# Performance work log

Hardware: AMD Instinct MI355X
Metric: run time of the kernel (lower is better)

The kernel has to match this reference:

```python
import jax, jax.numpy as jnp
import numpy as np

N_NODES = 50000
N_EDGES = 1_600_000
IN_DIM = 128
HID = 64


def gcn_conv(x, src, dst, w, W, b, n):
    # PyG GCNConv(normalize=True, add_self_loops=True):
    # add self loops with weight 1, sym-normalize, x@W (no bias in lin), scatter-add, +bias
    loop = jnp.arange(n)
    s = jnp.concatenate([src, loop])
    d = jnp.concatenate([dst, loop])
    ww = jnp.concatenate([w, jnp.ones((n,), w.dtype)])
    deg = jax.ops.segment_sum(ww, d, num_segments=n)                 # [n]
    dis = jnp.where(deg > 0, jax.lax.rsqrt(deg), 0.0)                # deg^{-1/2}, inf->0
    norm = dis[s] * ww * dis[d]                                      # [E+n]
    h = x @ W                                                        # [n, out]
    msg = h[s] * norm[:, None]                                       # gather + scale
    out = jax.ops.segment_sum(msg, d, num_segments=n)                # scatter-add at dst
    return out + b


def setup_inputs() -> dict:
    key = jax.random.key(0)
    ks = jax.random.split(key, 9)
    X = jax.random.normal(ks[0], (N_NODES, IN_DIM), dtype=jnp.float32)
    edge_index = jax.random.randint(ks[1], (2, N_EDGES), 0, N_NODES, dtype=jnp.int64)
    edge_weight = jax.random.uniform(ks[2], (N_EDGES,), dtype=jnp.float32)
    s1 = 1.0 / np.sqrt(IN_DIM)
    s2 = 1.0 / np.sqrt(HID)
    W1 = jax.random.uniform(ks[3], (IN_DIM, HID), jnp.float32, -s1, s1)
    b1 = jax.random.uniform(ks[4], (HID,), jnp.float32, -s1, s1)
    W2 = jax.random.uniform(ks[5], (HID, HID), jnp.float32, -s2, s2)
    b2 = jax.random.uniform(ks[6], (HID,), jnp.float32, -s2, s2)
    Wl = jax.random.uniform(ks[7], (HID, 1), jnp.float32, -s2, s2)
    bl = jax.random.uniform(ks[8], (1,), jnp.float32, -s2, s2)
    return {"X": X, "edge_index": edge_index, "edge_weight": edge_weight,
            "W1": W1, "b1": b1, "W2": W2, "b2": b2, "Wl": Wl, "bl": bl}


def reference(X, edge_index, edge_weight, W1, b1, W2, b2, Wl, bl):
    n = X.shape[0]
    src, dst = edge_index[0], edge_index[1]
    h = jax.nn.relu(gcn_conv(X, src, dst, edge_weight, W1, b1, n))
    # F.dropout(p=0.2) is identity in eval mode
    h = jax.nn.relu(gcn_conv(h, src, dst, edge_weight, W2, b2, n))
    return jax.nn.sigmoid(h @ Wl + bl).squeeze(1)   # [n]
```

## Files before the change

### kernel.cpp

```cpp
#include <hip/hip_runtime.h>

typedef float f32x2 __attribute__((ext_vector_type(2)));

#define A2B 512
#define A2T 512
#define STG 3200

__device__ __forceinline__ long ld_idx(const void* idx, long pos, int is64) {
  return is64 ? (long)((const long long*)idx)[pos]
              : (long)((const int*)idx)[pos];
}

__device__ __forceinline__ int detect_is64(const void* idx) {
  const unsigned long long* p = (const unsigned long long*)idx;
  unsigned long long v = p[threadIdx.x & 63];
  return (__ballot((v >> 32) != 0ull) == 0ull) ? 1 : 0;
}

__device__ __forceinline__ uint4 pack16_fp8(const float* acc) {
  uint4 o;
  unsigned v;
  v = 0;
  v = __builtin_amdgcn_cvt_pk_fp8_f32(acc[0],  acc[1],  v, false);
  v = __builtin_amdgcn_cvt_pk_fp8_f32(acc[2],  acc[3],  v, true);
  o.x = v; v = 0;
  v = __builtin_amdgcn_cvt_pk_fp8_f32(acc[4],  acc[5],  v, false);
  v = __builtin_amdgcn_cvt_pk_fp8_f32(acc[6],  acc[7],  v, true);
  o.y = v; v = 0;
  v = __builtin_amdgcn_cvt_pk_fp8_f32(acc[8],  acc[9],  v, false);
  v = __builtin_amdgcn_cvt_pk_fp8_f32(acc[10], acc[11], v, true);
  o.z = v; v = 0;
  v = __builtin_amdgcn_cvt_pk_fp8_f32(acc[12], acc[13], v, false);
  v = __builtin_amdgcn_cvt_pk_fp8_f32(acc[14], acc[15], v, true);
  o.w = v;
  return o;
}

__global__ __launch_bounds__(256) void k_front(const void* __restrict__ idx,
                                               unsigned* __restrict__ histT,
                                               long E, int chunk, unsigned M,
                                               const float* __restrict__ X,
                                               const float* __restrict__ W1,
                                               unsigned char* __restrict__ h, int n) {
  __shared__ float smem[2048];
  const int t = threadIdx.x;
  if (blockIdx.x < A2B) {
    unsigned* cnt = (unsigned*)smem;
    const int b = blockIdx.x;
    const int is64 = detect_is64(idx);
    cnt[t] = 0;
    __syncthreads();
    const long e0 = (long)b * chunk;
    long e1 = e0 + chunk; if (e1 > E) e1 = E;
    for (long e = e0 + t; e < e1; e += 256) {
      unsigned d = (unsigned)ld_idx(idx, E + e, is64);
      atomicAdd(&cnt[__umulhi(d, M)], 1u);
    }
    __syncthreads();
    histT[(size_t)t * A2B + b] = cnt[t];
    return;
  }
  float* Ws = smem;
  for (int i = t; i < 2048; i += 256)
    ((float4*)Ws)[i] = ((const float4*)W1)[i];
  __syncthreads();
  int gid = (blockIdx.x - A2B) * 256 + t;
  int node = gid >> 2;
  int fg = (gid & 3) * 16;
  if (node >= n) return;
  const float4* xr4 = (const float4*)(X + (size_t)node * 128);
  float acc[16];
#pragma unroll
  for (int f = 0; f < 16; ++f) acc[f] = 0.0f;
  for (int k4 = 0; k4 < 32; ++k4) {
    float4 x = xr4[k4];
#pragma unroll
    for (int kk = 0; kk < 4; ++kk) {
      float xv = (kk == 0) ? x.x : (kk == 1) ? x.y : (kk == 2) ? x.z : x.w;
      const float4* wrow = (const float4*)(Ws + (k4 * 4 + kk) * 64 + fg);
#pragma unroll
      for (int f4 = 0; f4 < 4; ++f4) {
        float4 w = wrow[f4];
        acc[f4 * 4 + 0] = fmaf(xv, w.x, acc[f4 * 4 + 0]);
        acc[f4 * 4 + 1] = fmaf(xv, w.y, acc[f4 * 4 + 1]);
        acc[f4 * 4 + 2] = fmaf(xv, w.z, acc[f4 * 4 + 2]);
        acc[f4 * 4 + 3] = fmaf(xv, w.w, acc[f4 * 4 + 3]);
      }
    }
  }
  *(uint4*)(h + (size_t)node * 64 + fg) = pack16_fp8(acc);
}

__global__ __launch_bounds__(256) void k_colscan(const unsigned* __restrict__ histT,
                                                 unsigned* __restrict__ baseT,
                                                 unsigned* __restrict__ colsum) {
  __shared__ unsigned sh[256];
  const int k = blockIdx.x, t = threadIdx.x;
  const uint2 v = ((const uint2*)(histT + (size_t)k * A2B))[t];
  unsigned s = v.x + v.y;
  sh[t] = s;
  __syncthreads();
  for (int off = 1; off < 256; off <<= 1) {
    unsigned u = (t >= off) ? sh[t - off] : 0;
    __syncthreads();
    sh[t] += u;
    __syncthreads();
  }
  unsigned excl = sh[t] - s;
  uint2 o; o.x = excl; o.y = excl + v.x;
  ((uint2*)(baseT + (size_t)k * A2B))[t] = o;
  if (t == 255) colsum[k] = sh[255];
}

__global__ __launch_bounds__(A2T) void k_bucket(const void* __restrict__ idx,
                                                const float* __restrict__ w,
                                                const unsigned* __restrict__ baseT,
                                                const unsigned* __restrict__ colsum,
                                                uint2* __restrict__ recs,
                                                long E, int chunk, unsigned M) {
  __shared__ uint2 stage[STG];
  __shared__ unsigned cnt[256], lofs[256], lbase[256], bcol[256], scanb[256];
  const int b = blockIdx.x, t = threadIdx.x;
  const long e0 = (long)b * chunk;
  long e1 = e0 + chunk; if (e1 > E) e1 = E;
  const int m = (int)(e1 - e0);
  const int is64 = detect_is64(idx);
  if (t < 256) scanb[t] = colsum[t];
  __syncthreads();
  for (int off = 1; off < 256; off <<= 1) {
    unsigned u = 0;
    if (t < 256 && t >= off) u = scanb[t - off];
    __syncthreads();
    if (t < 256) scanb[t] += u;
    __syncthreads();
  }
  if (t < 256) {
    bcol[t] = (scanb[t] - colsum[t]) + baseT[(size_t)t * A2B + b];
    cnt[t] = 0;
  }
  __syncthreads();
  unsigned short dc[8]; unsigned char kc[8];
  int nk = 0;
  for (long e = e0 + t; e < e1; e += A2T, ++nk) {
    unsigned d = (unsigned)ld_idx(idx, E + e, is64);
    unsigned kb = __umulhi(d, M);
    dc[nk] = (unsigned short)d; kc[nk] = (unsigned char)kb;
    atomicAdd(&cnt[kb], 1u);
  }
  __syncthreads();
  if (t < 256) scanb[t] = cnt[t];
  __syncthreads();
  for (int off = 1; off < 256; off <<= 1) {
    unsigned u = 0;
    if (t < 256 && t >= off) u = scanb[t - off];
    __syncthreads();
    if (t < 256) scanb[t] += u;
    __syncthreads();
  }
  if (t < 256) { unsigned ex = scanb[t] - cnt[t]; lbase[t] = ex; lofs[t] = ex; }
  __syncthreads();
  nk = 0;
  for (long e = e0 + t; e < e1; e += A2T, ++nk) {
    unsigned s = (unsigned)ld_idx(idx, e, is64);
    float wv = w[e];
    unsigned kb = kc[nk];
    unsigned pos = atomicAdd(&lofs[kb], 1u);
    stage[pos] = make_uint2(s | ((unsigned)dc[nk] << 16), __float_as_uint(wv));
  }
  __syncthreads();
  for (int i = t; i < m; i += A2T) {
    uint2 r = stage[i];
    unsigned kb = __umulhi(r.x >> 16, M);
    recs[bcol[kb] + (unsigned)i - lbase[kb]] = r;
  }
}

__global__ __launch_bounds__(1024) void k_build(const uint2* __restrict__ recs,
                                                const unsigned* __restrict__ colsum,
                                                int* __restrict__ rowptr,
                                                float* __restrict__ dis,
                                                float2* __restrict__ edges,
                                                int n, int dwidth, long E) {
  __shared__ float wsum[256];
  __shared__ unsigned cnt[256], lofs[256], scanb[256];
  __shared__ int shr0, shr1;
  const int k = blockIdx.x, t = threadIdx.x;
  const int d0 = k * dwidth;
  if (t < 256) scanb[t] = colsum[t];
  __syncthreads();
  for (int off = 1; off < 256; off <<= 1) {
    unsigned u = 0;
    if (t < 256 && t >= off) u = scanb[t - off];
    __syncthreads();
    if (t < 256) scanb[t] += u;
    __syncthreads();
  }
  if (t == k) { shr1 = (int)scanb[t]; shr0 = (int)(scanb[t] - colsum[t]); }
  if (t < 256) { wsum[t] = 0.0f; cnt[t] = 0; }
  __syncthreads();
  const int r0 = shr0, r1 = shr1;
  const int m = r1 - r0;
  for (int i = t; i < m; i += 1024) {
    uint2 r = recs[r0 + i];
    int dl = (int)(r.x >> 16) - d0;
    atomicAdd(&cnt[dl], 1u);
    atomicAdd(&wsum[dl], __uint_as_float(r.y));
  }
  __syncthreads();
  if (t < 256) scanb[t] = cnt[t];
  __syncthreads();
  for (int off = 1; off < 256; off <<= 1) {
    unsigned u = 0;
    if (t < 256 && t >= off) u = scanb[t - off];
    __syncthreads();
    if (t < 256) scanb[t] += u;
    __syncthreads();
  }
  if (t < 256) {
    unsigned ex = scanb[t] - cnt[t];
    lofs[t] = (unsigned)r0 + ex;
    int d = d0 + t;
    if (t < dwidth && d < n) {
      rowptr[d] = r0 + (int)ex;
      dis[d] = rsqrtf(1.0f + wsum[t]);
    }
  }
  if (k == gridDim.x - 1 && t == 0) rowptr[n] = (int)E;
  __syncthreads();
  for (int i = t; i < m; i += 1024) {
    uint2 r = recs[r0 + i];
    unsigned pos = atomicAdd(&lofs[(int)(r.x >> 16) - d0], 1u);
    edges[pos] = make_float2(__uint_as_float(r.x & 0xffffu), __uint_as_float(r.y));
  }
}

__device__ __forceinline__ void gather_acc(const unsigned char* __restrict__ h,
                                           const float* __restrict__ dis,
                                           const float2* __restrict__ edges,
                                           int beg, int end, float s0,
                                           int half, int l32, int fl, int eg,
                                           float* acc) {
#pragma unroll
  for (int i = 0; i < 8; ++i) acc[i] = 0.0f;
  for (int base = beg; base < end; base += 32) {
    int m = end - base; if (m > 32) m = 32;
    float2 pk = (l32 < m) ? edges[base + l32] : make_float2(__int_as_float(0), 0.0f);
    float nrm = dis[__float_as_int(pk.x)] * pk.y * s0;
    int steps = (m + 3) >> 2;
    for (int s = 0; s < steps; ++s) {
      int j = half * 32 + s * 4 + eg;
      int   sj = __float_as_int(__shfl(pk.x, j));
      float nj = __shfl(nrm, j);
      uint2 hv = *(const uint2*)(h + (size_t)sj * 64 + fl * 8);
      f32x2 p0 = __builtin_amdgcn_cvt_pk_f32_fp8(hv.x, false);
      f32x2 p1 = __builtin_amdgcn_cvt_pk_f32_fp8(hv.x, true);
      f32x2 p2 = __builtin_amdgcn_cvt_pk_f32_fp8(hv.y, false);
      f32x2 p3 = __builtin_amdgcn_cvt_pk_f32_fp8(hv.y, true);
      acc[0] = fmaf(p0[0], nj, acc[0]);
      acc[1] = fmaf(p0[1], nj, acc[1]);
      acc[2] = fmaf(p1[0], nj, acc[2]);
      acc[3] = fmaf(p1[1], nj, acc[3]);
      acc[4] = fmaf(p2[0], nj, acc[4]);
      acc[5] = fmaf(p2[1], nj, acc[5]);
      acc[6] = fmaf(p3[0], nj, acc[6]);
      acc[7] = fmaf(p3[1], nj, acc[7]);
    }
  }
#pragma unroll
  for (int off = 8; off < 32; off <<= 1)
#pragma unroll
    for (int i = 0; i < 8; ++i) acc[i] += __shfl_xor(acc[i], off);
}

__device__ __forceinline__ void add_bias_self(const unsigned char* __restrict__ h,
                                              const float* __restrict__ b,
                                              int node, int fl, float s0, float* acc) {
  uint2 hv = *(const uint2*)(h + (size_t)node * 64 + fl * 8);
  f32x2 q0 = __builtin_amdgcn_cvt_pk_f32_fp8(hv.x, false);
  f32x2 q1 = __builtin_amdgcn_cvt_pk_f32_fp8(hv.x, true);
  f32x2 q2 = __builtin_amdgcn_cvt_pk_f32_fp8(hv.y, false);
  f32x2 q3 = __builtin_amdgcn_cvt_pk_f32_fp8(hv.y, true);
  float hs[8] = {q0[0], q0[1], q1[0], q1[1], q2[0], q2[1], q3[0], q3[1]};
  float4 bv0 = *(const float4*)(b + fl * 8);
  float4 bv1 = *(const float4*)(b + fl * 8 + 4);
  float bb[8] = {bv0.x, bv0.y, bv0.z, bv0.w, bv1.x, bv1.y, bv1.z, bv1.w};
  float s2 = s0 * s0;
#pragma unroll
  for (int i = 0; i < 8; ++i) acc[i] += bb[i] + hs[i] * s2;
}

__global__ __launch_bounds__(256) void k_gather_mid(const unsigned char* __restrict__ h,
                                                    const float* __restrict__ dis,
                                                    const float2* __restrict__ edges,
                                                    const int* __restrict__ rowptr,
                                                    const float* __restrict__ b1,
                                                    const float* __restrict__ W2,
                                                    unsigned char* __restrict__ h2, int n) {
  __shared__ float W2s[64 * 64];
  __shared__ float xs[8 * 64];
  const int t = threadIdx.x;
  for (int i = t; i < 1024; i += 256)
    ((float4*)W2s)[i] = ((const float4*)W2)[i];
  int lane = t & 63;
  int half = lane >> 5;
  int l32 = lane & 31;
  int fl = lane & 7;
  int eg = (lane >> 3) & 3;
  int nl = t >> 5;
  int node = blockIdx.x * 8 + nl;
  int beg = 0, end = 0; float s0 = 0.0f;
  if (node < n) { beg = rowptr[node]; end = rowptr[node + 1]; s0 = dis[node]; }
  float acc[8];
  gather_acc(h, dis, edges, beg, end, s0, half, l32, fl, eg, acc);
  if (node < n) {
    add_bias_self(h, b1, node, fl, s0, acc);
    if (eg == 0) {
#pragma unroll
      for (int i = 0; i < 8; ++i) xs[nl * 64 + fl * 8 + i] = fmaxf(acc[i], 0.0f);
    }
  }
  __syncthreads();
  int tl = l32;
  int node2 = blockIdx.x * 8 + (t >> 5);
  if (node2 >= n) return;
  const float* xrow = xs + (t >> 5) * 64;
  int f = tl * 2;
  float a0 = 0.0f, a1 = 0.0f;
#pragma unroll 8
  for (int k = 0; k < 64; ++k) {
    float xk = xrow[k];
    f32x2 wv = *(const f32x2*)(W2s + k * 64 + f);
    a0 = fmaf(xk, wv[0], a0);
    a1 = fmaf(xk, wv[1], a1);
  }
  unsigned v = __builtin_amdgcn_cvt_pk_fp8_f32(a0, a1, 0u, false);
  *(unsigned short*)(h2 + (size_t)node2 * 64 + f) = (unsigned short)v;
}

__global__ __launch_bounds__(256) void k_gather_fin(const unsigned char* __restrict__ h,
                                                    const float* __restrict__ dis,
                                                    const float2* __restrict__ edges,
                                                    const int* __restrict__ rowptr,
                                                    const float* __restrict__ b2,
                                                    const float* __restrict__ Wl,
                                                    const float* __restrict__ bl,
                                                    float* __restrict__ out, int n) {
  int lane = threadIdx.x & 63;
  int half = lane >> 5;
  int l32 = lane & 31;
  int fl = lane & 7;
  int eg = (lane >> 3) & 3;
  int node = blockIdx.x * 8 + (int)(threadIdx.x >> 5);
  if (node >= n) return;
  int beg = rowptr[node], end = rowptr[node + 1];
  float s0 = dis[node];
  float acc[8];
  gather_acc(h, dis, edges, beg, end, s0, half, l32, fl, eg, acc);
  add_bias_self(h, b2, node, fl, s0, acc);
  float4 wl0 = *(const float4*)(Wl + fl * 8);
  float4 wl1 = *(const float4*)(Wl + fl * 8 + 4);
  float wl[8] = {wl0.x, wl0.y, wl0.z, wl0.w, wl1.x, wl1.y, wl1.z, wl1.w};
  float v = 0.0f;
#pragma unroll
  for (int i = 0; i < 8; ++i) v += fmaxf(acc[i], 0.0f) * wl[i];
#pragma unroll
  for (int off = 1; off < 8; off <<= 1) v += __shfl_xor(v, off);
  if (l32 == 0) out[node] = 1.0f / (1.0f + expf(-(v + bl[0])));
}

extern "C" void kernel_launch(void* const* d_in, const int* in_sizes, int n_in,
                              void* d_out, int out_size, void* d_ws, size_t ws_size,
                              hipStream_t stream) {
  const float* X  = (const float*)d_in[0];
  const void*  EI = d_in[1];
  const float* EW = (const float*)d_in[2];
  const float* W1 = (const float*)d_in[3];
  const float* b1 = (const float*)d_in[4];
  const float* W2 = (const float*)d_in[5];
  const float* b2 = (const float*)d_in[6];
  const float* Wl = (const float*)d_in[7];
  const float* bl = (const float*)d_in[8];
  float* out = (float*)d_out;

  const int  n = in_sizes[0] / 128;
  const long E = (long)in_sizes[1] / 2;

  const int chunk  = (int)((E + A2B - 1) / A2B);
  const int dwidth = (n + 255) / 256;
  const unsigned M = (unsigned)((0x100000000ULL + (unsigned)dwidth - 1) / (unsigned)dwidth);

  auto align = [](size_t x) { return (x + 255) & ~(size_t)255; };
  char* ws = (char*)d_ws;
  size_t off = 0;
  float*         dis    = (float*)(ws + off);         off += align((size_t)n * 4);
  int*           rowptr = (int*)(ws + off);           off += align((size_t)(n + 1) * 4);
  unsigned*      colsum = (unsigned*)(ws + off);      off += align(256 * 4);
  unsigned*      histT  = (unsigned*)(ws + off);      off += align((size_t)A2B * 256 * 4);
  unsigned*      baseT  = (unsigned*)(ws + off);      off += align((size_t)A2B * 256 * 4);
  uint2*         recs   = (uint2*)(ws + off);         off += align((size_t)E * 8);
  float2*        edges  = (float2*)(ws + off);        off += align((size_t)E * 8);
  unsigned char* A      = (unsigned char*)(ws + off); off += align((size_t)n * 64);
  unsigned char* A2     = (unsigned char*)(ws + off); off += align((size_t)n * 64);

  const int nbW = (n + 7) / 8;
  const int nbG = (n * 4 + 255) / 256;

  k_front<<<A2B + nbG, dim3(256), 0, stream>>>(EI, histT, E, chunk, M, X, W1, A, n);
  k_colscan<<<256, 256, 0, stream>>>(histT, baseT, colsum);
  k_bucket<<<A2B, A2T, 0, stream>>>(EI, EW, baseT, colsum, recs, E, chunk, M);
  k_build<<<256, 1024, 0, stream>>>(recs, colsum, rowptr, dis, edges, n, dwidth, E);

  k_gather_mid<<<nbW, dim3(256), 0, stream>>>(A, dis, edges, rowptr, b1, W2, A2, n);
  k_gather_fin<<<nbW, dim3(256), 0, stream>>>(A2, dis, edges, rowptr, b2, Wl, bl, out, n);
}
```

Measured before the change: 211.7 us.

## Split layer-2 GEMM out of gather kernel into separate fp8 GEMM kernel

After: 218.2 us. +3.1%, slower.

```diff
diff --git a/kernel.cpp b/kernel.cpp
--- a/kernel.cpp
+++ b/kernel.cpp
@@ -294,47 +294,68 @@
                                                     const float2* __restrict__ edges,
                                                     const int* __restrict__ rowptr,
                                                     const float* __restrict__ b1,
-                                                    const float* __restrict__ W2,
-                                                    unsigned char* __restrict__ h2, int n) {
-  __shared__ float W2s[64 * 64];
-  __shared__ float xs[8 * 64];
-  const int t = threadIdx.x;
-  for (int i = t; i < 1024; i += 256)
-    ((float4*)W2s)[i] = ((const float4*)W2)[i];
-  int lane = t & 63;
+                                                    unsigned char* __restrict__ x1, int n) {
+  int lane = threadIdx.x & 63;
   int half = lane >> 5;
   int l32 = lane & 31;
   int fl = lane & 7;
   int eg = (lane >> 3) & 3;
-  int nl = t >> 5;
-  int node = blockIdx.x * 8 + nl;
-  int beg = 0, end = 0; float s0 = 0.0f;
-  if (node < n) { beg = rowptr[node]; end = rowptr[node + 1]; s0 = dis[node]; }
+  int node = blockIdx.x * 8 + (int)(threadIdx.x >> 5);
+  if (node >= n) return;
+  int beg = rowptr[node], end = rowptr[node + 1];
+  float s0 = dis[node];
   float acc[8];
   gather_acc(h, dis, edges, beg, end, s0, half, l32, fl, eg, acc);
-  if (node < n) {
+  if (eg == 0) {
     add_bias_self(h, b1, node, fl, s0, acc);
-    if (eg == 0) {
-#pragma unroll
-      for (int i = 0; i < 8; ++i) xs[nl * 64 + fl * 8 + i] = fmaxf(acc[i], 0.0f);
+#pragma unroll
+    for (int i = 0; i < 8; ++i) acc[i] = fmaxf(acc[i], 0.0f);
+    unsigned w0 = 0, w1 = 0;
+    w0 = __builtin_amdgcn_cvt_pk_fp8_f32(acc[0], acc[1], w0, false);
+    w0 = __builtin_amdgcn_cvt_pk_fp8_f32(acc[2], acc[3], w0, true);
+    w1 = __builtin_amdgcn_cvt_pk_fp8_f32(acc[4], acc[5], w1, false);
+    w1 = __builtin_amdgcn_cvt_pk_fp8_f32(acc[6], acc[7], w1, true);
+    *(uint2*)(x1 + (size_t)node * 64 + fl * 8) = make_uint2(w0, w1);
+  }
+}
+
+__global__ __launch_bounds__(256) void k_gemm2b(const unsigned char* __restrict__ x1,
+                                                const float* __restrict__ W2,
+                                                unsigned char* __restrict__ h2, int n) {
+  __shared__ float Ws[64 * 64];
+  for (int i = threadIdx.x; i < 1024; i += 256)
+    ((float4*)Ws)[i] = ((const float4*)W2)[i];
+  __syncthreads();
+  int gid = blockIdx.x * 256 + threadIdx.x;
+  int node = gid >> 2;
+  int fg = (gid & 3) * 16;
+  if (node >= n) return;
+  const uint4* xr = (const uint4*)(x1 + (size_t)node * 64);
+  uint4 rw[4] = {xr[0], xr[1], xr[2], xr[3]};
+  const unsigned* words = (const unsigned*)rw;
+  float acc[16];
+#pragma unroll
+  for (int f = 0; f < 16; ++f) acc[f] = 0.0f;
+#pragma unroll 4
+  for (int w = 0; w < 16; ++w) {
+    f32x2 a = __builtin_amdgcn_cvt_pk_f32_fp8(words[w], false);
+    f32x2 c = __builtin_amdgcn_cvt_pk_f32_fp8(words[w], true);
+    float xv4[4] = {a[0], a[1], c[0], c[1]};
+#pragma unroll
+    for (int j = 0; j < 4; ++j) {
+      float xv = xv4[j];
+      const float4* wrow = (const float4*)(Ws + (w * 4 + j) * 64 + fg);
+#pragma unroll
+      for (int f4 = 0; f4 < 4; ++f4) {
+        float4 wv = wrow[f4];
+        acc[f4 * 4 + 0] = fmaf(xv, wv.x, acc[f4 * 4 + 0]);
+        acc[f4 * 4 + 1] = fmaf(xv, wv.y, acc[f4 * 4 + 1]);
+        acc[f4 * 4 + 2] = fmaf(xv, wv.z, acc[f4 * 4 + 2]);
+        acc[f4 * 4 + 3] = fmaf(xv, wv.w, acc[f4 * 4 + 3]);
+      }
     }
   }
-  __syncthreads();
-  int tl = l32;
-  int node2 = blockIdx.x * 8 + (t >> 5);
-  if (node2 >= n) return;
-  const float* xrow = xs + (t >> 5) * 64;
-  int f = tl * 2;
-  float a0 = 0.0f, a1 = 0.0f;
-#pragma unroll 8
-  for (int k = 0; k < 64; ++k) {
-    float xk = xrow[k];
-    f32x2 wv = *(const f32x2*)(W2s + k * 64 + f);
-    a0 = fmaf(xk, wv[0], a0);
-    a1 = fmaf(xk, wv[1], a1);
-  }
-  unsigned v = __builtin_amdgcn_cvt_pk_fp8_f32(a0, a1, 0u, false);
-  *(unsigned short*)(h2 + (size_t)node2 * 64 + f) = (unsigned short)v;
+  *(uint4*)(h2 + (size_t)node * 64 + fg) = pack16_fp8(acc);
 }
 
 __global__ __launch_bounds__(256) void k_gather_fin(const unsigned char* __restrict__ h,
@@ -400,6 +421,7 @@
   uint2*         recs   = (uint2*)(ws + off);         off += align((size_t)E * 8);
   float2*        edges  = (float2*)(ws + off);        off += align((size_t)E * 8);
   unsigned char* A      = (unsigned char*)(ws + off); off += align((size_t)n * 64);
+  unsigned char* X1     = (unsigned char*)(ws + off); off += align((size_t)n * 64);
   unsigned char* A2     = (unsigned char*)(ws + off); off += align((size_t)n * 64);
 
   const int nbW = (n + 7) / 8;
@@ -410,6 +432,7 @@
   k_bucket<<<A2B, A2T, 0, stream>>>(EI, EW, baseT, colsum, recs, E, chunk, M);
   k_build<<<256, 1024, 0, stream>>>(recs, colsum, rowptr, dis, edges, n, dwidth, E);
 
-  k_gather_mid<<<nbW, dim3(256), 0, stream>>>(A, dis, edges, rowptr, b1, W2, A2, n);
+  k_gather_mid<<<nbW, dim3(256), 0, stream>>>(A, dis, edges, rowptr, b1, X1, n);
+  k_gemm2b<<<nbG, dim3(256), 0, stream>>>(X1, W2, A2, n);
   k_gather_fin<<<nbW, dim3(256), 0, stream>>>(A2, dis, edges, rowptr, b2, Wl, bl, out, n);
 }
```

## Reorder second GCN layer to aggregate first then apply W2

Applied to the files above, without the earlier changes.

Result: slower. 221.3 us (+4.5%).

```diff
diff --git a/kernel.cpp b/kernel.cpp
--- a/kernel.cpp
+++ b/kernel.cpp
@@ -272,21 +272,17 @@
     for (int i = 0; i < 8; ++i) acc[i] += __shfl_xor(acc[i], off);
 }
 
-__device__ __forceinline__ void add_bias_self(const unsigned char* __restrict__ h,
-                                              const float* __restrict__ b,
-                                              int node, int fl, float s0, float* acc) {
+__device__ __forceinline__ void add_self(const unsigned char* __restrict__ h,
+                                         int node, int fl, float s0, float* acc) {
   uint2 hv = *(const uint2*)(h + (size_t)node * 64 + fl * 8);
   f32x2 q0 = __builtin_amdgcn_cvt_pk_f32_fp8(hv.x, false);
   f32x2 q1 = __builtin_amdgcn_cvt_pk_f32_fp8(hv.x, true);
   f32x2 q2 = __builtin_amdgcn_cvt_pk_f32_fp8(hv.y, false);
   f32x2 q3 = __builtin_amdgcn_cvt_pk_f32_fp8(hv.y, true);
   float hs[8] = {q0[0], q0[1], q1[0], q1[1], q2[0], q2[1], q3[0], q3[1]};
-  float4 bv0 = *(const float4*)(b + fl * 8);
-  float4 bv1 = *(const float4*)(b + fl * 8 + 4);
-  float bb[8] = {bv0.x, bv0.y, bv0.z, bv0.w, bv1.x, bv1.y, bv1.z, bv1.w};
   float s2 = s0 * s0;
 #pragma unroll
-  for (int i = 0; i < 8; ++i) acc[i] += bb[i] + hs[i] * s2;
+  for (int i = 0; i < 8; ++i) acc[i] += hs[i] * s2;
 }
 
 __global__ __launch_bounds__(256) void k_gather_mid(const unsigned char* __restrict__ h,
@@ -294,57 +290,7 @@
                                                     const float2* __restrict__ edges,
                                                     const int* __restrict__ rowptr,
                                                     const float* __restrict__ b1,
-                                                    const float* __restrict__ W2,
-                                                    unsigned char* __restrict__ h2, int n) {
-  __shared__ float W2s[64 * 64];
-  __shared__ float xs[8 * 64];
-  const int t = threadIdx.x;
-  for (int i = t; i < 1024; i += 256)
-    ((float4*)W2s)[i] = ((const float4*)W2)[i];
-  int lane = t & 63;
-  int half = lane >> 5;
-  int l32 = lane & 31;
-  int fl = lane & 7;
-  int eg = (lane >> 3) & 3;
-  int nl = t >> 5;
-  int node = blockIdx.x * 8 + nl;
-  int beg = 0, end = 0; float s0 = 0.0f;
-  if (node < n) { beg = rowptr[node]; end = rowptr[node + 1]; s0 = dis[node]; }
-  float acc[8];
-  gather_acc(h, dis, edges, beg, end, s0, half, l32, fl, eg, acc);
-  if (node < n) {
-    add_bias_self(h, b1, node, fl, s0, acc);
-    if (eg == 0) {
-#pragma unroll
-      for (int i = 0; i < 8; ++i) xs[nl * 64 + fl * 8 + i] = fmaxf(acc[i], 0.0f);
-    }
-  }
-  __syncthreads();
-  int tl = l32;
-  int node2 = blockIdx.x * 8 + (t >> 5);
-  if (node2 >= n) return;
-  const float* xrow = xs + (t >> 5) * 64;
-  int f = tl * 2;
-  float a0 = 0.0f, a1 = 0.0f;
-#pragma unroll 8
-  for (int k = 0; k < 64; ++k) {
-    float xk = xrow[k];
-    f32x2 wv = *(const f32x2*)(W2s + k * 64 + f);
-    a0 = fmaf(xk, wv[0], a0);
-    a1 = fmaf(xk, wv[1], a1);
-  }
-  unsigned v = __builtin_amdgcn_cvt_pk_fp8_f32(a0, a1, 0u, false);
-  *(unsigned short*)(h2 + (size_t)node2 * 64 + f) = (unsigned short)v;
-}
-
-__global__ __launch_bounds__(256) void k_gather_fin(const unsigned char* __restrict__ h,
-                                                    const float* __restrict__ dis,
-                                                    const float2* __restrict__ edges,
-                                                    const int* __restrict__ rowptr,
-                                                    const float* __restrict__ b2,
-                                                    const float* __restrict__ Wl,
-                                                    const float* __restrict__ bl,
-                                                    float* __restrict__ out, int n) {
+                                                    unsigned char* __restrict__ x1, int n) {
   int lane = threadIdx.x & 63;
   int half = lane >> 5;
   int l32 = lane & 31;
@@ -356,15 +302,66 @@
   float s0 = dis[node];
   float acc[8];
   gather_acc(h, dis, edges, beg, end, s0, half, l32, fl, eg, acc);
-  add_bias_self(h, b2, node, fl, s0, acc);
-  float4 wl0 = *(const float4*)(Wl + fl * 8);
-  float4 wl1 = *(const float4*)(Wl + fl * 8 + 4);
-  float wl[8] = {wl0.x, wl0.y, wl0.z, wl0.w, wl1.x, wl1.y, wl1.z, wl1.w};
-  float v = 0.0f;
-#pragma unroll
-  for (int i = 0; i < 8; ++i) v += fmaxf(acc[i], 0.0f) * wl[i];
-#pragma unroll
-  for (int off = 1; off < 8; off <<= 1) v += __shfl_xor(v, off);
+  if (eg == 0) {
+    add_self(h, node, fl, s0, acc);
+    float4 bv0 = *(const float4*)(b1 + fl * 8);
+    float4 bv1 = *(const float4*)(b1 + fl * 8 + 4);
+    float bb[8] = {bv0.x, bv0.y, bv0.z, bv0.w, bv1.x, bv1.y, bv1.z, bv1.w};
+#pragma unroll
+    for (int i = 0; i < 8; ++i) acc[i] = fmaxf(acc[i] + bb[i], 0.0f);
+    unsigned w0 = 0, w1 = 0;
+    w0 = __builtin_amdgcn_cvt_pk_fp8_f32(acc[0], acc[1], w0, false);
+    w0 = __builtin_amdgcn_cvt_pk_fp8_f32(acc[2], acc[3], w0, true);
+    w1 = __builtin_amdgcn_cvt_pk_fp8_f32(acc[4], acc[5], w1, false);
+    w1 = __builtin_amdgcn_cvt_pk_fp8_f32(acc[6], acc[7], w1, true);
+    *(uint2*)(x1 + (size_t)node * 64 + fl * 8) = make_uint2(w0, w1);
+  }
+}
+
+__global__ __launch_bounds__(256) void k_gather_fin(const unsigned char* __restrict__ x1,
+                                                    const float* __restrict__ dis,
+                                                    const float2* __restrict__ edges,
+                                                    const int* __restrict__ rowptr,
+                                                    const float* __restrict__ W2,
+                                                    const float* __restrict__ b2,
+                                                    const float* __restrict__ Wl,
+                                                    const float* __restrict__ bl,
+                                                    float* __restrict__ out, int n) {
+  __shared__ float W2s[64 * 64];
+  const int t = threadIdx.x;
+  for (int i = t; i < 1024; i += 256)
+    ((float4*)W2s)[i] = ((const float4*)W2)[i];
+  __syncthreads();
+
+  int lane = t & 63;
+  int half = lane >> 5;
+  int l32 = lane & 31;
+  int fl = lane & 7;
+  int eg = (lane >> 3) & 3;
+  int node = blockIdx.x * 8 + (int)(t >> 5);
+  if (node >= n) return;
+  int beg = rowptr[node], end = rowptr[node + 1];
+  float s0 = dis[node];
+  float acc[8];
+  gather_acc(x1, dis, edges, beg, end, s0, half, l32, fl, eg, acc);
+  add_self(x1, node, fl, s0, acc);
+  const int f = l32 * 2;
+  float z0 = 0.0f, z1 = 0.0f;
+#pragma unroll
+  for (int kg = 0; kg < 8; ++kg) {
+#pragma unroll
+    for (int i = 0; i < 8; ++i) {
+      float ak = __shfl(acc[i], half * 32 + kg);
+      f32x2 wv = *(const f32x2*)(W2s + (kg * 8 + i) * 64 + f);
+      z0 = fmaf(ak, wv[0], z0);
+      z1 = fmaf(ak, wv[1], z1);
+    }
+  }
+  f32x2 b2v = *(const f32x2*)(b2 + f);
+  f32x2 wlv = *(const f32x2*)(Wl + f);
+  float v = fmaxf(z0 + b2v[0], 0.0f) * wlv[0] + fmaxf(z1 + b2v[1], 0.0f) * wlv[1];
+#pragma unroll
+  for (int off = 1; off < 32; off <<= 1) v += __shfl_xor(v, off);
   if (l32 == 0) out[node] = 1.0f / (1.0f + expf(-(v + bl[0])));
 }
 
@@ -400,7 +397,7 @@
   uint2*         recs   = (uint2*)(ws + off);         off += align((size_t)E * 8);
   float2*        edges  = (float2*)(ws + off);        off += align((size_t)E * 8);
   unsigned char* A      = (unsigned char*)(ws + off); off += align((size_t)n * 64);
-  unsigned char* A2     = (unsigned char*)(ws + off); off += align((size_t)n * 64);
+  unsigned char* X1     = (unsigned char*)(ws + off); off += align((size_t)n * 64);
 
   const int nbW = (n + 7) / 8;
   const int nbG = (n * 4 + 255) / 256;
@@ -410,6 +407,6 @@
   k_bucket<<<A2B, A2T, 0, stream>>>(EI, EW, baseT, colsum, recs, E, chunk, M);
   k_build<<<256, 1024, 0, stream>>>(recs, colsum, rowptr, dis, edges, n, dwidth, E);
 
-  k_gather_mid<<<nbW, dim3(256), 0, stream>>>(A, dis, edges, rowptr, b1, W2, A2, n);
-  k_gather_fin<<<nbW, dim3(256), 0, stream>>>(A2, dis, edges, rowptr, b2, Wl, bl, out, n);
-}
+  k_gather_mid<<<nbW, dim3(256), 0, stream>>>(A, dis, edges, rowptr, b1, X1, n);
+  k_gather_fin<<<nbW, dim3(256), 0, stream>>>(X1, dis, edges, rowptr, W2, b2, Wl, bl, out, n);
+}
```
